# Kernel optimization log

Measured on AMD Instinct MI355X. Metric: run time of the kernel, lower is better.

## Reference

```python
import jax, jax.numpy as jnp
import numpy as np

N = 50000        # nodes
E = 1_600_000    # edges
R = 4            # relations
F_IN = 32        # input_size
H1 = 32          # 8 * multiplier
H2 = 64          # 16 * multiplier
NC = 3           # num_classes
G = 64           # graphs in batch


def setup_inputs() -> dict:
    key = jax.random.key(0)
    ks = jax.random.split(key, 16)
    s = 0.1
    x = jax.random.normal(ks[0], (N, F_IN), jnp.float32)
    edge_index = jax.random.randint(ks[1], (2, E), 0, N, dtype=jnp.int32)
    edge_type = jax.random.randint(ks[2], (E,), 0, R, dtype=jnp.int32)
    batch = jnp.sort(jax.random.randint(ks[3], (N,), 0, G, dtype=jnp.int32))
    return {
        "x": x,
        "edge_index": edge_index,
        "edge_type": edge_type,
        "batch": batch,
        # RGCNConv 1: per-relation weights, root weight, bias
        "W1_rel": jax.random.normal(ks[4], (R, F_IN, H1), jnp.float32) * s,
        "W1_root": jax.random.normal(ks[5], (F_IN, H1), jnp.float32) * s,
        "b1": jax.random.normal(ks[6], (H1,), jnp.float32) * s,
        # RGCNConv 2
        "W2_rel": jax.random.normal(ks[7], (R, H1, H2), jnp.float32) * s,
        "W2_root": jax.random.normal(ks[8], (H1, H2), jnp.float32) * s,
        "b2": jax.random.normal(ks[9], (H2,), jnp.float32) * s,
        # MLP head (stored as (in, out))
        "lin1_w": jax.random.normal(ks[10], (H2, H1), jnp.float32) * s,
        "lin1_b": jax.random.normal(ks[11], (H1,), jnp.float32) * s,
        "lin2_w": jax.random.normal(ks[12], (H1, NC), jnp.float32) * s,
        "lin2_b": jax.random.normal(ks[13], (NC,), jnp.float32) * s,
    }


def _rgcn_layer(x, src, dst, edge_type, W_rel, W_root, b):
    # PyG RGCNConv: out_i = x_i @ W_root + b + sum_r mean_{j in N_r(i)} x_j @ W_r
    out = x @ W_root + b
    for r in range(R):  # small fixed relation count
        h = x @ W_rel[r]                       # [N, out] dense transform once per relation
        mask = (edge_type == r)
        msg = jnp.where(mask[:, None], h[src], 0.0)          # [E, out] masked gather
        agg = jax.ops.segment_sum(msg, dst, num_segments=N)  # [N, out]
        cnt = jax.ops.segment_sum(mask.astype(x.dtype), dst, num_segments=N)
        out = out + agg / jnp.maximum(cnt, 1.0)[:, None]     # mean aggregation
    return out


def reference(x, edge_index, edge_type, batch, W1_rel, W1_root, b1,
              W2_rel, W2_root, b2, lin1_w, lin1_b, lin2_w, lin2_b):
    src, dst = edge_index[0], edge_index[1]
    h = jax.nn.relu(_rgcn_layer(x, src, dst, edge_type, W1_rel, W1_root, b1))
    h = jax.nn.relu(_rgcn_layer(h, src, dst, edge_type, W2_rel, W2_root, b2))
    g = jax.ops.segment_max(h, batch, num_segments=G)        # global_max_pool -> [G, H2]
    g = jnp.where(jnp.isneginf(g), 0.0, g)                   # empty-graph guard
    g = jax.nn.relu(g @ lin1_w + lin1_b)
    return g @ lin2_w + lin2_b
```

## Files before the change

### kernel.cpp

```cpp
#include <hip/hip_runtime.h>

#define N_NODES 50000
#define N_EDGES 1600000
#define R_REL 4
#define F_IN 32
#define H1 32
#define H2 64
#define NC 3
#define G_BATCH 64
#define BKT 196
#define CHUNK 6400
#define NBIN (N_EDGES / CHUNK)
#define SENTINEL (R_REL << 16)

__global__ __launch_bounds__(256) void bcount_kernel(const int* __restrict__ dstp,
                                                     int* __restrict__ bucketCnt) {
    __shared__ int h[BKT];
    for (int i = threadIdx.x; i < BKT; i += 256) h[i] = 0;
    __syncthreads();
    int e0 = blockIdx.x * CHUNK;
    for (int e = e0 + threadIdx.x; e < e0 + CHUNK; e += 256)
        atomicAdd(&h[dstp[e] >> 8], 1);
    __syncthreads();
    for (int i = threadIdx.x; i < BKT; i += 256)
        if (h[i]) atomicAdd(&bucketCnt[i], h[i]);
}

__global__ __launch_bounds__(256) void bscan_kernel(const int* __restrict__ bucketCnt,
                                                    int* __restrict__ bucketOff,
                                                    int* __restrict__ bucketCursor) {
    __shared__ int s[256];
    int v = (threadIdx.x < BKT) ? bucketCnt[threadIdx.x] : 0;
    s[threadIdx.x] = v;
    __syncthreads();
    for (int w = 1; w < 256; w <<= 1) {
        int t = (threadIdx.x >= w) ? s[threadIdx.x - w] : 0;
        __syncthreads();
        s[threadIdx.x] += t;
        __syncthreads();
    }
    if (threadIdx.x < BKT) {
        int o = s[threadIdx.x] - v;
        bucketOff[threadIdx.x] = o;
        bucketCursor[threadIdx.x] = o;
    }
}

__global__ __launch_bounds__(256) void bin_kernel(const int* __restrict__ srcp,
                                                  const int* __restrict__ dstp,
                                                  const int* __restrict__ etype,
                                                  int* __restrict__ bucketCursor,
                                                  int* __restrict__ binned) {
    __shared__ int h[BKT];
    __shared__ int lc[BKT];
    for (int i = threadIdx.x; i < BKT; i += 256) { h[i] = 0; lc[i] = 0; }
    __syncthreads();
    int e0 = blockIdx.x * CHUNK;
    for (int e = e0 + threadIdx.x; e < e0 + CHUNK; e += 256)
        atomicAdd(&h[dstp[e] >> 8], 1);
    __syncthreads();
    for (int i = threadIdx.x; i < BKT; i += 256) {
        int c = h[i];
        h[i] = c ? atomicAdd(&bucketCursor[i], c) : 0;
    }
    __syncthreads();
    for (int e = e0 + threadIdx.x; e < e0 + CHUNK; e += 256) {
        int d = dstp[e];
        int b = d >> 8;
        int rank = atomicAdd(&lc[b], 1);
        binned[h[b] + rank] = srcp[e] | (etype[e] << 16) | ((d & 0xFF) << 18);
    }
}

__global__ __launch_bounds__(256) void bcnt2_kernel(const int* __restrict__ binned,
                                                    const int* __restrict__ bucketOff,
                                                    const int* __restrict__ bucketCnt,
                                                    float* __restrict__ inv,
                                                    int* __restrict__ deg,
                                                    int* __restrict__ partial) {
    __shared__ int cnt4[256 * R_REL];
    __shared__ int s[256];
    for (int i = threadIdx.x; i < 256 * R_REL; i += 256) cnt4[i] = 0;
    __syncthreads();
    int b = blockIdx.x;
    int i0 = bucketOff[b], i1 = i0 + bucketCnt[b];
    for (int i = i0 + threadIdx.x; i < i1; i += 256) {
        int p = binned[i];
        atomicAdd(&cnt4[((p >> 18) & 0xFF) * R_REL + ((p >> 16) & 3)], 1);
    }
    __syncthreads();
    int n = b * 256 + threadIdx.x;
    int d = 0;
    if (n < N_NODES) {
#pragma unroll
        for (int r = 0; r < R_REL; ++r) {
            int cr = cnt4[threadIdx.x * R_REL + r];
            d += cr;
            inv[r * N_NODES + n] = 1.0f / (float)(cr > 1 ? cr : 1);
        }
        deg[n] = d;
    }
    s[threadIdx.x] = d;
    __syncthreads();
    for (int w = 128; w > 0; w >>= 1) {
        if (threadIdx.x < w) s[threadIdx.x] += s[threadIdx.x + w];
        __syncthreads();
    }
    if (threadIdx.x == 0) partial[b] = s[0];
}

__global__ __launch_bounds__(256) void scanB_kernel(int* __restrict__ partial) {
    __shared__ int s[256];
    int v = (threadIdx.x < BKT) ? partial[threadIdx.x] : 0;
    s[threadIdx.x] = v;
    __syncthreads();
    for (int w = 1; w < 256; w <<= 1) {
        int t = (threadIdx.x >= w) ? s[threadIdx.x - w] : 0;
        __syncthreads();
        s[threadIdx.x] += t;
        __syncthreads();
    }
    if (threadIdx.x < BKT) partial[threadIdx.x] = s[threadIdx.x] - v;
}

__global__ __launch_bounds__(256) void scanC_kernel(const int* __restrict__ deg,
                                                    const int* __restrict__ partial,
                                                    int* __restrict__ off) {
    __shared__ int s[256];
    int n = blockIdx.x * 256 + threadIdx.x;
    int d = (n < N_NODES) ? deg[n] : 0;
    s[threadIdx.x] = d;
    __syncthreads();
    for (int w = 1; w < 256; w <<= 1) {
        int t = (threadIdx.x >= w) ? s[threadIdx.x - w] : 0;
        __syncthreads();
        s[threadIdx.x] += t;
        __syncthreads();
    }
    if (n < N_NODES) off[n] = partial[blockIdx.x] + s[threadIdx.x] - d;
}

__global__ __launch_bounds__(256) void bscatter_kernel(const int* __restrict__ binned,
                                                       const int* __restrict__ bucketOff,
                                                       const int* __restrict__ bucketCnt,
                                                       const int* __restrict__ off,
                                                       int* __restrict__ elist) {
    __shared__ int cur[256];
    int b = blockIdx.x;
    int n = b * 256 + threadIdx.x;
    cur[threadIdx.x] = (n < N_NODES) ? off[n] : 0;
    __syncthreads();
    int i0 = bucketOff[b], i1 = i0 + bucketCnt[b];
    for (int i = i0 + threadIdx.x; i < i1; i += 256) {
        int p = binned[i];
        int pos = atomicAdd(&cur[(p >> 18) & 0xFF], 1);
        elist[pos] = p & 0x3FFFF;
    }
}

__global__ __launch_bounds__(256, 6) void layer1_kernel(
    const float* __restrict__ x, const int* __restrict__ off,
    const int* __restrict__ deg, const int* __restrict__ elist,
    const float* __restrict__ inv, const float* __restrict__ W_rel,
    const float* __restrict__ W_root, const float* __restrict__ b,
    float* __restrict__ h1) {
    __shared__ float sxr[8][F_IN];
    __shared__ float sagg[8][R_REL][F_IN];

    int ln = threadIdx.x >> 5, c = threadIdx.x & 31;
    int n = blockIdx.x * 8 + ln;
    if (n >= N_NODES) return;

    sxr[ln][c] = x[n * F_IN + c];
    float a0 = 0.f, a1 = 0.f, a2 = 0.f, a3 = 0.f;
    int e0 = off[n], e1 = e0 + deg[n];
    for (int eb = e0; eb < e1; eb += 32) {
        int idx = eb + c;
        int pv = (idx < e1) ? elist[idx] : SENTINEL;
#pragma unroll
        for (int j0 = 0; j0 < 32; j0 += 8) {
#pragma unroll
            for (int j = j0; j < j0 + 8; ++j) {
                int p = __shfl(pv, j, 32);
                float v = x[(p & 0xFFFF) * F_IN + c];
                int r = p >> 16;
                a0 += (r == 0) ? v : 0.0f;
                a1 += (r == 1) ? v : 0.0f;
                a2 += (r == 2) ? v : 0.0f;
                a3 += (r == 3) ? v : 0.0f;
            }
        }
    }
    sagg[ln][0][c] = a0 * inv[0 * N_NODES + n];
    sagg[ln][1][c] = a1 * inv[1 * N_NODES + n];
    sagg[ln][2][c] = a2 * inv[2 * N_NODES + n];
    sagg[ln][3][c] = a3 * inv[3 * N_NODES + n];

    float o = b[c];
#pragma unroll
    for (int i = 0; i < F_IN; ++i)
        o = fmaf(sxr[ln][i], W_root[i * H1 + c], o);
#pragma unroll
    for (int r = 0; r < R_REL; ++r)
#pragma unroll
        for (int i = 0; i < F_IN; ++i)
            o = fmaf(sagg[ln][r][i], W_rel[r * F_IN * H1 + i * H1 + c], o);
    h1[n * H1 + c] = fmaxf(o, 0.0f);
}

__global__ __launch_bounds__(256, 6) void layer2_kernel(
    const float* __restrict__ h1, const int* __restrict__ off,
    const int* __restrict__ deg, const int* __restrict__ elist,
    const float* __restrict__ inv, const float* __restrict__ W_rel,
    const float* __restrict__ W_root, const float* __restrict__ b,
    float* __restrict__ out2) {
    __shared__ float sxr[8][H1];
    __shared__ float sagg[8][R_REL][H1];

    int ln = threadIdx.x >> 5, c = threadIdx.x & 31;
    int n = blockIdx.x * 8 + ln;
    if (n >= N_NODES) return;

    sxr[ln][c] = h1[n * H1 + c];
    float a0 = 0.f, a1 = 0.f, a2 = 0.f, a3 = 0.f;
    int e0 = off[n], e1 = e0 + deg[n];
    for (int eb = e0; eb < e1; eb += 32) {
        int idx = eb + c;
        int pv = (idx < e1) ? elist[idx] : SENTINEL;
#pragma unroll
        for (int j0 = 0; j0 < 32; j0 += 8) {
#pragma unroll
            for (int j = j0; j < j0 + 8; ++j) {
                int p = __shfl(pv, j, 32);
                float v = h1[(p & 0xFFFF) * H1 + c];
                int r = p >> 16;
                a0 += (r == 0) ? v : 0.0f;
                a1 += (r == 1) ? v : 0.0f;
                a2 += (r == 2) ? v : 0.0f;
                a3 += (r == 3) ? v : 0.0f;
            }
        }
    }
    sagg[ln][0][c] = a0 * inv[0 * N_NODES + n];
    sagg[ln][1][c] = a1 * inv[1 * N_NODES + n];
    sagg[ln][2][c] = a2 * inv[2 * N_NODES + n];
    sagg[ln][3][c] = a3 * inv[3 * N_NODES + n];

    float o0 = b[c], o1 = b[c + 32];
#pragma unroll
    for (int i = 0; i < H1; ++i) {
        float xv = sxr[ln][i];
        o0 = fmaf(xv, W_root[i * H2 + c], o0);
        o1 = fmaf(xv, W_root[i * H2 + c + 32], o1);
    }
#pragma unroll
    for (int r = 0; r < R_REL; ++r)
#pragma unroll
        for (int i = 0; i < H1; ++i) {
            float av = sagg[ln][r][i];
            o0 = fmaf(av, W_rel[r * H1 * H2 + i * H2 + c], o0);
            o1 = fmaf(av, W_rel[r * H1 * H2 + i * H2 + c + 32], o1);
        }
    out2[n * H2 + c] = o0;
    out2[n * H2 + c + 32] = o1;
}

#define POOL_NODES 32
__global__ __launch_bounds__(64) void pool_kernel(
    const float* __restrict__ out2, const int* __restrict__ batch,
    unsigned int* __restrict__ g) {
    int col = threadIdx.x;
    int n0 = blockIdx.x * POOL_NODES;
    if (n0 >= N_NODES) return;
    int n1 = n0 + POOL_NODES;
    if (n1 > N_NODES) n1 = N_NODES;
    int cur = batch[n0];
    float m = 0.0f;
    for (int n = n0; n < n1; ++n) {
        int bnow = batch[n];
        if (bnow != cur) {
            atomicMax(&g[cur * H2 + col], __float_as_uint(m));
            cur = bnow;
            m = 0.0f;
        }
        m = fmaxf(m, out2[n * H2 + col]);
    }
    atomicMax(&g[cur * H2 + col], __float_as_uint(m));
}

__global__ __launch_bounds__(256) void mlp_kernel(
    const unsigned int* __restrict__ gbits, const float* __restrict__ lin1_w,
    const float* __restrict__ lin1_b, const float* __restrict__ lin2_w,
    const float* __restrict__ lin2_b, float* __restrict__ out) {
    __shared__ float sg[G_BATCH][H2];
    __shared__ float sh[G_BATCH][H1];
    __shared__ float sw1[H2 * H1];
    for (int i = threadIdx.x; i < G_BATCH * H2; i += 256)
        sg[i / H2][i % H2] = __uint_as_float(gbits[i]);
    for (int i = threadIdx.x; i < H2 * H1; i += 256) sw1[i] = lin1_w[i];
    __syncthreads();
    for (int i = threadIdx.x; i < G_BATCH * H1; i += 256) {
        int gi = i / H1, c = i % H1;
        float a = lin1_b[c];
#pragma unroll
        for (int k = 0; k < H2; ++k) a = fmaf(sg[gi][k], sw1[k * H1 + c], a);
        sh[gi][c] = fmaxf(a, 0.0f);
    }
    __syncthreads();
    for (int i = threadIdx.x; i < G_BATCH * NC; i += 256) {
        int gi = i / NC, c = i % NC;
        float a = lin2_b[c];
#pragma unroll
        for (int k = 0; k < H1; ++k) a = fmaf(sh[gi][k], lin2_w[k * NC + c], a);
        out[gi * NC + c] = a;
    }
}

extern "C" void kernel_launch(void* const* d_in, const int* in_sizes, int n_in,
                              void* d_out, int out_size, void* d_ws, size_t ws_size,
                              hipStream_t stream) {
    const float* x       = (const float*)d_in[0];
    const int*   eidx    = (const int*)d_in[1];
    const int*   etype   = (const int*)d_in[2];
    const int*   batch   = (const int*)d_in[3];
    const float* W1_rel  = (const float*)d_in[4];
    const float* W1_root = (const float*)d_in[5];
    const float* b1      = (const float*)d_in[6];
    const float* W2_rel  = (const float*)d_in[7];
    const float* W2_root = (const float*)d_in[8];
    const float* b2      = (const float*)d_in[9];
    const float* lin1_w  = (const float*)d_in[10];
    const float* lin1_b  = (const float*)d_in[11];
    const float* lin2_w  = (const float*)d_in[12];
    const float* lin2_b  = (const float*)d_in[13];
    const int* srcp = eidx;
    const int* dstp = eidx + N_EDGES;

    char* ws = (char*)d_ws;
    size_t o = 0;
    int*      bucketCnt    = (int*)(ws + o);   o += (size_t)256 * 4;
    int*      bucketOff    = (int*)(ws + o);   o += (size_t)256 * 4;
    int*      bucketCursor = (int*)(ws + o);   o += (size_t)256 * 4;
    int*      partial      = (int*)(ws + o);   o += (size_t)256 * 4;
    float*    inv          = (float*)(ws + o); o += (size_t)R_REL * N_NODES * 4;
    int*      degv         = (int*)(ws + o);   o += (size_t)N_NODES * 4;
    int*      offv         = (int*)(ws + o);   o += (size_t)N_NODES * 4;
    int*      binned       = (int*)(ws + o);   o += (size_t)N_EDGES * 4;
    int*      elist        = (int*)(ws + o);   o += (size_t)N_EDGES * 4;
    unsigned* g            = (unsigned*)(ws + o); o += (size_t)G_BATCH * H2 * 4;
    float*    h1           = (float*)(ws + o); o += (size_t)N_NODES * H1 * 4;
    float*    out2         = (float*)(ws + o); o += (size_t)N_NODES * H2 * 4;

    hipMemsetAsync(bucketCnt, 0, 256 * 4, stream);
    hipMemsetAsync(g, 0, (size_t)G_BATCH * H2 * 4, stream);

    bcount_kernel<<<NBIN, 256, 0, stream>>>(dstp, bucketCnt);
    bscan_kernel<<<1, 256, 0, stream>>>(bucketCnt, bucketOff, bucketCursor);
    bin_kernel<<<NBIN, 256, 0, stream>>>(srcp, dstp, etype, bucketCursor, binned);
    bcnt2_kernel<<<BKT, 256, 0, stream>>>(binned, bucketOff, bucketCnt, inv, degv,
                                          partial);
    scanB_kernel<<<1, 256, 0, stream>>>(partial);
    scanC_kernel<<<BKT, 256, 0, stream>>>(degv, partial, offv);
    bscatter_kernel<<<BKT, 256, 0, stream>>>(binned, bucketOff, bucketCnt, offv,
                                             elist);

    layer1_kernel<<<(N_NODES + 7) / 8, 256, 0, stream>>>(
        x, offv, degv, elist, inv, W1_rel, W1_root, b1, h1);
    layer2_kernel<<<(N_NODES + 7) / 8, 256, 0, stream>>>(
        h1, offv, degv, elist, inv, W2_rel, W2_root, b2, out2);

    pool_kernel<<<(N_NODES + POOL_NODES - 1) / POOL_NODES, 64, 0, stream>>>(
        out2, batch, g);
    mlp_kernel<<<1, 256, 0, stream>>>(g, lin1_w, lin1_b, lin2_w, lin2_b,
                                      (float*)d_out);
}
```

Baseline: 358.8 us.

## Sort edges by node and relation into padded segments to drop per-edge relation selects

```diff
diff --git a/kernel.cpp b/kernel.cpp
--- a/kernel.cpp
+++ b/kernel.cpp
@@ -11,7 +11,16 @@
 #define BKT 196
 #define CHUNK 6400
 #define NBIN (N_EDGES / CHUNK)
-#define SENTINEL (R_REL << 16)
+#define ELIST_CAP (N_EDGES + N_NODES * R_REL * 8)
+
+__global__ __launch_bounds__(256) void copyx_kernel(const float* __restrict__ x,
+                                                    float* __restrict__ xp,
+                                                    float* __restrict__ h1zero) {
+    int i = blockIdx.x * 256 + threadIdx.x;
+    if (i < (N_NODES + 1) * F_IN)
+        xp[i] = (i < N_NODES * F_IN) ? x[i] : 0.0f;
+    if (i < H1) h1zero[i] = 0.0f;
+}
 
 __global__ __launch_bounds__(256) void bcount_kernel(const int* __restrict__ dstp,
                                                      int* __restrict__ bucketCnt) {
@@ -76,7 +85,7 @@
                                                     const int* __restrict__ bucketOff,
                                                     const int* __restrict__ bucketCnt,
                                                     float* __restrict__ inv,
-                                                    int* __restrict__ deg,
+                                                    int* __restrict__ rcnt4,
                                                     int* __restrict__ partial) {
     __shared__ int cnt4[256 * R_REL];
     __shared__ int s[256];
@@ -92,13 +101,18 @@
     int n = b * 256 + threadIdx.x;
     int d = 0;
     if (n < N_NODES) {
-#pragma unroll
-        for (int r = 0; r < R_REL; ++r) {
-            int cr = cnt4[threadIdx.x * R_REL + r];
-            d += cr;
-            inv[r * N_NODES + n] = 1.0f / (float)(cr > 1 ? cr : 1);
-        }
-        deg[n] = d;
+        int4 w;
+        int c0 = cnt4[threadIdx.x * 4 + 0];
+        int c1 = cnt4[threadIdx.x * 4 + 1];
+        int c2 = cnt4[threadIdx.x * 4 + 2];
+        int c3 = cnt4[threadIdx.x * 4 + 3];
+        inv[0 * N_NODES + n] = 1.0f / (float)(c0 > 1 ? c0 : 1);
+        inv[1 * N_NODES + n] = 1.0f / (float)(c1 > 1 ? c1 : 1);
+        inv[2 * N_NODES + n] = 1.0f / (float)(c2 > 1 ? c2 : 1);
+        inv[3 * N_NODES + n] = 1.0f / (float)(c3 > 1 ? c3 : 1);
+        w.x = c0; w.y = c1; w.z = c2; w.w = c3;
+        *(int4*)&rcnt4[n * 4] = w;
+        d = ((c0 + 7) & ~7) + ((c1 + 7) & ~7) + ((c2 + 7) & ~7) + ((c3 + 7) & ~7);
     }
     s[threadIdx.x] = d;
     __syncthreads();
@@ -123,12 +137,20 @@
     if (threadIdx.x < BKT) partial[threadIdx.x] = s[threadIdx.x] - v;
 }
 
-__global__ __launch_bounds__(256) void scanC_kernel(const int* __restrict__ deg,
+__global__ __launch_bounds__(256) void scanC_kernel(const int* __restrict__ rcnt4,
                                                     const int* __restrict__ partial,
-                                                    int* __restrict__ off) {
+                                                    int* __restrict__ poff4) {
     __shared__ int s[256];
     int n = blockIdx.x * 256 + threadIdx.x;
-    int d = (n < N_NODES) ? deg[n] : 0;
+    int p0 = 0, p1 = 0, p2 = 0, p3 = 0, d = 0;
+    if (n < N_NODES) {
+        int4 rc = *(const int4*)&rcnt4[n * 4];
+        p0 = (rc.x + 7) & ~7;
+        p1 = (rc.y + 7) & ~7;
+        p2 = (rc.z + 7) & ~7;
+        p3 = (rc.w + 7) & ~7;
+        d = p0 + p1 + p2 + p3;
+    }
     s[threadIdx.x] = d;
     __syncthreads();
     for (int w = 1; w < 256; w <<= 1) {
@@ -137,30 +159,56 @@
         s[threadIdx.x] += t;
         __syncthreads();
     }
-    if (n < N_NODES) off[n] = partial[blockIdx.x] + s[threadIdx.x] - d;
+    if (n < N_NODES) {
+        int base = partial[blockIdx.x] + s[threadIdx.x] - d;
+        int4 w;
+        w.x = base;
+        w.y = base + p0;
+        w.z = base + p0 + p1;
+        w.w = base + p0 + p1 + p2;
+        *(int4*)&poff4[n * 4] = w;
+    }
 }
 
 __global__ __launch_bounds__(256) void bscatter_kernel(const int* __restrict__ binned,
                                                        const int* __restrict__ bucketOff,
                                                        const int* __restrict__ bucketCnt,
-                                                       const int* __restrict__ off,
+                                                       const int* __restrict__ poff4,
+                                                       const int* __restrict__ rcnt4,
                                                        int* __restrict__ elist) {
-    __shared__ int cur[256];
-    int b = blockIdx.x;
-    int n = b * 256 + threadIdx.x;
-    cur[threadIdx.x] = (n < N_NODES) ? off[n] : 0;
+    __shared__ int cur[256 * 4];
+    int b = blockIdx.x, t = threadIdx.x;
+    int n = b * 256 + t;
+    int4 po = make_int4(0, 0, 0, 0);
+    if (n < N_NODES) po = *(const int4*)&poff4[n * 4];
+    cur[t * 4 + 0] = po.x;
+    cur[t * 4 + 1] = po.y;
+    cur[t * 4 + 2] = po.z;
+    cur[t * 4 + 3] = po.w;
     __syncthreads();
     int i0 = bucketOff[b], i1 = i0 + bucketCnt[b];
-    for (int i = i0 + threadIdx.x; i < i1; i += 256) {
+    for (int i = i0 + t; i < i1; i += 256) {
         int p = binned[i];
-        int pos = atomicAdd(&cur[(p >> 18) & 0xFF], 1);
-        elist[pos] = p & 0x3FFFF;
-    }
-}
-
-__global__ __launch_bounds__(256, 6) void layer1_kernel(
-    const float* __restrict__ x, const int* __restrict__ off,
-    const int* __restrict__ deg, const int* __restrict__ elist,
+        int pos = atomicAdd(&cur[((p >> 18) & 0xFF) * 4 + ((p >> 16) & 3)], 1);
+        elist[pos] = p & 0xFFFF;
+    }
+    __syncthreads();
+    if (n < N_NODES) {
+        int4 rc = *(const int4*)&rcnt4[n * 4];
+        int rcv[4] = {rc.x, rc.y, rc.z, rc.w};
+        int pov[4] = {po.x, po.y, po.z, po.w};
+#pragma unroll
+        for (int r = 0; r < R_REL; ++r) {
+            int e = cur[t * 4 + r];
+            int pe = pov[r] + ((rcv[r] + 7) & ~7);
+            for (; e < pe; ++e) elist[e] = N_NODES;
+        }
+    }
+}
+
+__global__ __launch_bounds__(256, 8) void layer1_kernel(
+    const float* __restrict__ xp, const int* __restrict__ poff4,
+    const int* __restrict__ rcnt4, const int* __restrict__ elist,
     const float* __restrict__ inv, const float* __restrict__ W_rel,
     const float* __restrict__ W_root, const float* __restrict__ b,
     float* __restrict__ h1) {
@@ -171,30 +219,30 @@
     int n = blockIdx.x * 8 + ln;
     if (n >= N_NODES) return;
 
-    sxr[ln][c] = x[n * F_IN + c];
-    float a0 = 0.f, a1 = 0.f, a2 = 0.f, a3 = 0.f;
-    int e0 = off[n], e1 = e0 + deg[n];
-    for (int eb = e0; eb < e1; eb += 32) {
-        int idx = eb + c;
-        int pv = (idx < e1) ? elist[idx] : SENTINEL;
-#pragma unroll
-        for (int j0 = 0; j0 < 32; j0 += 8) {
-#pragma unroll
-            for (int j = j0; j < j0 + 8; ++j) {
-                int p = __shfl(pv, j, 32);
-                float v = x[(p & 0xFFFF) * F_IN + c];
-                int r = p >> 16;
-                a0 += (r == 0) ? v : 0.0f;
-                a1 += (r == 1) ? v : 0.0f;
-                a2 += (r == 2) ? v : 0.0f;
-                a3 += (r == 3) ? v : 0.0f;
+    sxr[ln][c] = xp[n * F_IN + c];
+    int4 po = *(const int4*)&poff4[n * 4];
+    int4 rc = *(const int4*)&rcnt4[n * 4];
+    int pov[4] = {po.x, po.y, po.z, po.w};
+    int rcv[4] = {rc.x, rc.y, rc.z, rc.w};
+    int c7 = c & 7;
+#pragma unroll
+    for (int r = 0; r < R_REL; ++r) {
+        int sb = pov[r];
+        int pc = (rcv[r] + 7) & ~7;
+        float a = 0.0f;
+        for (int eb = 0; eb < pc; eb += 8) {
+            int pv = elist[sb + eb + c7];
+            float v[8];
+#pragma unroll
+            for (int j = 0; j < 8; ++j) {
+                int p = __shfl(pv, j, 8);
+                v[j] = xp[p * F_IN + c];
             }
+#pragma unroll
+            for (int j = 0; j < 8; ++j) a += v[j];
         }
-    }
-    sagg[ln][0][c] = a0 * inv[0 * N_NODES + n];
-    sagg[ln][1][c] = a1 * inv[1 * N_NODES + n];
-    sagg[ln][2][c] = a2 * inv[2 * N_NODES + n];
-    sagg[ln][3][c] = a3 * inv[3 * N_NODES + n];
+        sagg[ln][r][c] = a * inv[r * N_NODES + n];
+    }
 
     float o = b[c];
 #pragma unroll
@@ -208,9 +256,9 @@
     h1[n * H1 + c] = fmaxf(o, 0.0f);
 }
 
-__global__ __launch_bounds__(256, 6) void layer2_kernel(
-    const float* __restrict__ h1, const int* __restrict__ off,
-    const int* __restrict__ deg, const int* __restrict__ elist,
+__global__ __launch_bounds__(256, 8) void layer2_kernel(
+    const float* __restrict__ h1, const int* __restrict__ poff4,
+    const int* __restrict__ rcnt4, const int* __restrict__ elist,
     const float* __restrict__ inv, const float* __restrict__ W_rel,
     const float* __restrict__ W_root, const float* __restrict__ b,
     float* __restrict__ out2) {
@@ -222,29 +270,29 @@
     if (n >= N_NODES) return;
 
     sxr[ln][c] = h1[n * H1 + c];
-    float a0 = 0.f, a1 = 0.f, a2 = 0.f, a3 = 0.f;
-    int e0 = off[n], e1 = e0 + deg[n];
-    for (int eb = e0; eb < e1; eb += 32) {
-        int idx = eb + c;
-        int pv = (idx < e1) ? elist[idx] : SENTINEL;
-#pragma unroll
-        for (int j0 = 0; j0 < 32; j0 += 8) {
-#pragma unroll
-            for (int j = j0; j < j0 + 8; ++j) {
-                int p = __shfl(pv, j, 32);
-                float v = h1[(p & 0xFFFF) * H1 + c];
-                int r = p >> 16;
-                a0 += (r == 0) ? v : 0.0f;
-                a1 += (r == 1) ? v : 0.0f;
-                a2 += (r == 2) ? v : 0.0f;
-                a3 += (r == 3) ? v : 0.0f;
+    int4 po = *(const int4*)&poff4[n * 4];
+    int4 rc = *(const int4*)&rcnt4[n * 4];
+    int pov[4] = {po.x, po.y, po.z, po.w};
+    int rcv[4] = {rc.x, rc.y, rc.z, rc.w};
+    int c7 = c & 7;
+#pragma unroll
+    for (int r = 0; r < R_REL; ++r) {
+        int sb = pov[r];
+        int pc = (rcv[r] + 7) & ~7;
+        float a = 0.0f;
+        for (int eb = 0; eb < pc; eb += 8) {
+            int pv = elist[sb + eb + c7];
+            float v[8];
+#pragma unroll
+            for (int j = 0; j < 8; ++j) {
+                int p = __shfl(pv, j, 8);
+                v[j] = h1[p * H1 + c];
             }
+#pragma unroll
+            for (int j = 0; j < 8; ++j) a += v[j];
         }
-    }
-    sagg[ln][0][c] = a0 * inv[0 * N_NODES + n];
-    sagg[ln][1][c] = a1 * inv[1 * N_NODES + n];
-    sagg[ln][2][c] = a2 * inv[2 * N_NODES + n];
-    sagg[ln][3][c] = a3 * inv[3 * N_NODES + n];
+        sagg[ln][r][c] = a * inv[r * N_NODES + n];
+    }
 
     float o0 = b[c], o1 = b[c + 32];
 #pragma unroll
@@ -343,31 +391,34 @@
     int*      bucketCursor = (int*)(ws + o);   o += (size_t)256 * 4;
     int*      partial      = (int*)(ws + o);   o += (size_t)256 * 4;
     float*    inv          = (float*)(ws + o); o += (size_t)R_REL * N_NODES * 4;
-    int*      degv         = (int*)(ws + o);   o += (size_t)N_NODES * 4;
-    int*      offv         = (int*)(ws + o);   o += (size_t)N_NODES * 4;
+    int*      rcnt4        = (int*)(ws + o);   o += (size_t)R_REL * N_NODES * 4;
+    int*      poff4        = (int*)(ws + o);   o += (size_t)R_REL * N_NODES * 4;
     int*      binned       = (int*)(ws + o);   o += (size_t)N_EDGES * 4;
-    int*      elist        = (int*)(ws + o);   o += (size_t)N_EDGES * 4;
+    int*      elist        = (int*)(ws + o);   o += (size_t)ELIST_CAP * 4;
     unsigned* g            = (unsigned*)(ws + o); o += (size_t)G_BATCH * H2 * 4;
-    float*    h1           = (float*)(ws + o); o += (size_t)N_NODES * H1 * 4;
+    float*    xp           = (float*)(ws + o); o += (size_t)(N_NODES + 1) * F_IN * 4;
+    float*    h1           = (float*)(ws + o); o += (size_t)(N_NODES + 1) * H1 * 4;
     float*    out2         = (float*)(ws + o); o += (size_t)N_NODES * H2 * 4;
 
     hipMemsetAsync(bucketCnt, 0, 256 * 4, stream);
     hipMemsetAsync(g, 0, (size_t)G_BATCH * H2 * 4, stream);
 
+    copyx_kernel<<<((N_NODES + 1) * F_IN + 255) / 256, 256, 0, stream>>>(
+        x, xp, h1 + (size_t)N_NODES * H1);
     bcount_kernel<<<NBIN, 256, 0, stream>>>(dstp, bucketCnt);
     bscan_kernel<<<1, 256, 0, stream>>>(bucketCnt, bucketOff, bucketCursor);
     bin_kernel<<<NBIN, 256, 0, stream>>>(srcp, dstp, etype, bucketCursor, binned);
-    bcnt2_kernel<<<BKT, 256, 0, stream>>>(binned, bucketOff, bucketCnt, inv, degv,
-                                          partial);
+    bcnt2_kernel<<<BKT, 256, 0, stream>>>(binned, bucketOff, bucketCnt, inv,
+                                          rcnt4, partial);
     scanB_kernel<<<1, 256, 0, stream>>>(partial);
-    scanC_kernel<<<BKT, 256, 0, stream>>>(degv, partial, offv);
-    bscatter_kernel<<<BKT, 256, 0, stream>>>(binned, bucketOff, bucketCnt, offv,
-                                             elist);
+    scanC_kernel<<<BKT, 256, 0, stream>>>(rcnt4, partial, poff4);
+    bscatter_kernel<<<BKT, 256, 0, stream>>>(binned, bucketOff, bucketCnt, poff4,
+                                             rcnt4, elist);
 
     layer1_kernel<<<(N_NODES + 7) / 8, 256, 0, stream>>>(
-        x, offv, degv, elist, inv, W1_rel, W1_root, b1, h1);
+        xp, poff4, rcnt4, elist, inv, W1_rel, W1_root, b1, h1);
     layer2_kernel<<<(N_NODES + 7) / 8, 256, 0, stream>>>(
-        h1, offv, degv, elist, inv, W2_rel, W2_root, b2, out2);
+        h1, poff4, rcnt4, elist, inv, W2_rel, W2_root, b2, out2);
 
     pool_kernel<<<(N_NODES + POOL_NODES - 1) / POOL_NODES, 64, 0, stream>>>(
         out2, batch, g);
```

New measurement: 320.1 us. 10.8% less time.
